# Performance work log

Hardware: AMD Instinct MI355X
Metric: run time of the kernel (lower is better)

The kernel has to match this reference:

```python
import jax, jax.numpy as jnp
import numpy as np

N, E = 50000, 800000
DIM_IN, DIM_H, DIM_OUT, HEADS = 128, 32, 16, 4
HID = DIM_H * HEADS  # 128
FINAL = DIM_OUT * HEADS  # 64
NEG_SLOPE = 0.2


def _glorot(key, shape):
    fan_in, fan_out = shape[0], shape[-1] if len(shape) > 1 else shape[0]
    lim = jnp.sqrt(6.0 / (fan_in + fan_out)).astype(jnp.float32)
    return jax.random.uniform(key, shape, jnp.float32, -lim, lim)


def setup_inputs() -> dict:
    key = jax.random.key(0)
    ks = jax.random.split(key, 16)
    x = jax.random.normal(ks[0], (N, DIM_IN), jnp.float32)
    edge_index = jax.random.randint(ks[1], (2, E), 0, N, dtype=jnp.int64)
    inp = {"x": x, "edge_index": edge_index}
    # layer 1: DIM_IN -> HEADS*DIM_H
    inp["Wl1"] = _glorot(ks[2], (DIM_IN, HEADS * DIM_H))
    inp["Wr1"] = _glorot(ks[3], (DIM_IN, HEADS * DIM_H))
    inp["att1"] = _glorot(ks[4], (HEADS, DIM_H))
    inp["b1"] = jnp.zeros((HEADS * DIM_H,), jnp.float32)
    # layer 2: HID -> HEADS*DIM_H
    inp["Wl2"] = _glorot(ks[5], (HID, HEADS * DIM_H))
    inp["Wr2"] = _glorot(ks[6], (HID, HEADS * DIM_H))
    inp["att2"] = _glorot(ks[7], (HEADS, DIM_H))
    inp["b2"] = jnp.zeros((HEADS * DIM_H,), jnp.float32)
    # layer 3: HID -> HEADS*DIM_OUT
    inp["Wl3"] = _glorot(ks[8], (HID, HEADS * DIM_OUT))
    inp["Wr3"] = _glorot(ks[9], (HID, HEADS * DIM_OUT))
    inp["att3"] = _glorot(ks[10], (HEADS, DIM_OUT))
    inp["b3"] = jnp.zeros((HEADS * DIM_OUT,), jnp.float32)
    return inp


def gatv2_conv(x, src, dst, Wl, Wr, att, b, heads, ch):
    n = x.shape[0]
    xl = (x @ Wl).reshape(n, heads, ch)  # source-side transform
    xr = (x @ Wr).reshape(n, heads, ch)  # target-side transform
    m = xl[src] + xr[dst]                 # [E, H, C]
    e = jnp.einsum('ehc,hc->eh', jax.nn.leaky_relu(m, NEG_SLOPE), att)
    # segment softmax over incoming edges of each dst node
    emax = jax.ops.segment_max(e, dst, num_segments=n)
    ex = jnp.exp(e - emax[dst])
    denom = jax.ops.segment_sum(ex, dst, num_segments=n)
    alpha = ex / denom[dst]               # [E, H]
    out = jax.ops.segment_sum(alpha[:, :, None] * xl[src], dst, num_segments=n)
    return out.reshape(n, heads * ch) + b


def reference(x, edge_index, Wl1, Wr1, att1, b1, Wl2, Wr2, att2, b2, Wl3, Wr3, att3, b3):
    n = x.shape[0]
    loops = jnp.arange(n, dtype=edge_index.dtype)
    src = jnp.concatenate([edge_index[0], loops])  # PyG add_self_loops=True
    dst = jnp.concatenate([edge_index[1], loops])
    # dropout is identity in eval mode
    h = jax.nn.elu(gatv2_conv(x, src, dst, Wl1, Wr1, att1, b1, HEADS, DIM_H))
    h = jax.nn.elu(gatv2_conv(h, src, dst, Wl2, Wr2, att2, b2, HEADS, DIM_H))
    h = gatv2_conv(h, src, dst, Wl3, Wr3, att3, b3, HEADS, DIM_OUT)
    return jax.nn.log_softmax(h, axis=1)
```

## Files before the change

kernel.cpp:

```cpp
#include <hip/hip_runtime.h>
#include <math.h>

constexpr int DIN  = 128;
constexpr int FSH  = 10;
constexpr int NFBM = 64;
constexpr int LCAP = 160;
constexpr int RND  = 4096;
constexpr int FCAP = 18432;

typedef __attribute__((ext_vector_type(8))) short short8;
typedef __attribute__((ext_vector_type(4))) float f32x4;

__device__ __forceinline__ unsigned short f2bf(float f) {
  unsigned u = __float_as_uint(f);
  u = (u + 0x7FFF + ((u >> 16) & 1)) >> 16;
  return (unsigned short)u;
}
__device__ __forceinline__ float bflo(unsigned u) { return __uint_as_float(u << 16); }
__device__ __forceinline__ float bfhi(unsigned u) { return __uint_as_float(u & 0xFFFF0000u); }

__device__ __forceinline__ void unpack8(uint4 u, float* x) {
  x[0] = bflo(u.x); x[1] = bfhi(u.x); x[2] = bflo(u.y); x[3] = bfhi(u.y);
  x[4] = bflo(u.z); x[5] = bfhi(u.z); x[6] = bflo(u.w); x[7] = bfhi(u.w);
}
__device__ __forceinline__ void unpack4(uint2 u, float* x) {
  x[0] = bflo(u.x); x[1] = bfhi(u.x); x[2] = bflo(u.y); x[3] = bfhi(u.y);
}

typedef const __attribute__((address_space(1))) unsigned int guint_t;
typedef __attribute__((address_space(3))) unsigned int luint_t;
__device__ __forceinline__ void async16(const void* g, void* l) {
  __builtin_amdgcn_global_load_lds((guint_t*)g, (luint_t*)l, 16, 0, 0);
}


__global__ __launch_bounds__(256) void bucket_append_kernel(const int* __restrict__ ei,
    int* __restrict__ gcnt, unsigned* __restrict__ gpairs, int E, int nfb) {
  __shared__ unsigned buf[NFBM * LCAP];
  __shared__ int cnt[NFBM];
  __shared__ int gbase[NFBM];
  const int tid = threadIdx.x;
  if (tid < NFBM) cnt[tid] = 0;
  __syncthreads();

  const int k0 = blockIdx.x * RND;
  for (int i = tid; i < RND; i += 256) {
    int k = k0 + i;
    if (k >= E) break;
    int src = ei[k], dst = ei[E + k];
    int fb = dst >> FSH;
    int pos = atomicAdd(&cnt[fb], 1);
    if (pos < LCAP)
      buf[fb * LCAP + pos] = (unsigned)src | ((unsigned)(dst & ((1 << FSH) - 1)) << 16);
  }
  __syncthreads();

  if (tid < nfb) gbase[tid] = atomicAdd(&gcnt[tid], min(cnt[tid], LCAP));
  __syncthreads();

  const int wid = tid >> 6, lane = tid & 63;
  for (int fb = wid; fb < nfb; fb += 4) {
    int c  = min(cnt[fb], LCAP);
    int gb = gbase[fb];
    if (gb >= FCAP) continue;
    c = min(c, FCAP - gb);
    unsigned* dstp = gpairs + (size_t)fb * FCAP + gb;
    const unsigned* srcp = &buf[fb * LCAP];
    for (int i = lane; i < c; i += 64) dstp[i] = srcp[i];
  }
}

__global__ __launch_bounds__(256) void bucket_build_kernel(const unsigned* __restrict__ gpairs,
    const int* __restrict__ gcnt, int* __restrict__ row_ptr,
    int* __restrict__ edge_src, int n, int nfb) {
  const int b   = blockIdx.x;
  const int tid = threadIdx.x;
  const int lane = tid & 63, wid = tid >> 6;
  __shared__ int hist[1024];
  __shared__ int wsum[4];
  __shared__ int base_s;

  const int d0 = b << FSH;
  const int nvalid = min(1 << FSH, n - d0);

  if (tid == 0) {
    int s = 0;
    for (int i = 0; i < b; ++i)
      s += min(gcnt[i], FCAP) + min(1 << FSH, n - (i << FSH));
    base_s = s;
  }
  for (int i = tid; i < 1024; i += 256) hist[i] = (i < nvalid) ? 1 : 0;
  __syncthreads();

  const int cnt = min(gcnt[b], FCAP);
  const unsigned* bp = gpairs + (size_t)b * FCAP;
  for (int i = tid; i < cnt; i += 256)
    atomicAdd(&hist[bp[i] >> 16], 1);
  __syncthreads();

  const int i4 = tid * 4;
  int h0 = hist[i4], h1 = hist[i4 + 1], h2 = hist[i4 + 2], h3 = hist[i4 + 3];
  int s = h0 + h1 + h2 + h3;
  int incl = s;
#pragma unroll
  for (int o = 1; o < 64; o <<= 1) {
    int t = __shfl_up(incl, o, 64);
    if (lane >= o) incl += t;
  }
  if (lane == 63) wsum[wid] = incl;
  __syncthreads();
  int wo = 0;
  for (int wq = 0; wq < wid; ++wq) wo += wsum[wq];
  const int base = base_s;
  int ex[4];
  ex[0] = wo + incl - s;
  ex[1] = ex[0] + h0;
  ex[2] = ex[1] + h1;
  ex[3] = ex[2] + h2;
#pragma unroll
  for (int j = 0; j < 4; ++j) {
    int d = i4 + j;
    if (d < nvalid) {
      row_ptr[d0 + d] = base + ex[j];
      edge_src[base + ex[j]] = d0 + d;
      hist[d] = ex[j] + 1;
    } else if (d0 + d == n) {
      row_ptr[n] = base + ex[j];
    }
  }
  if (b == nfb - 1 && d0 + 1024 <= n && tid == 0) row_ptr[n] = base + cnt + nvalid;
  __syncthreads();

  for (int i = tid; i < cnt; i += 256) {
    unsigned p = bp[i];
    int pos = atomicAdd(&hist[p >> 16], 1);
    edge_src[base + pos] = (int)(p & 0xFFFFu);
  }
}


__global__ __launch_bounds__(256) void cvt_x_kernel(const float* __restrict__ x,
                                                    unsigned short* __restrict__ xb, int total4) {
  int i = blockIdx.x * 256 + threadIdx.x;
  if (i >= total4) return;
  float4 v = *(const float4*)&x[i * 4];
  uint2 o;
  o.x = (unsigned)f2bf(v.x) | ((unsigned)f2bf(v.y) << 16);
  o.y = (unsigned)f2bf(v.z) | ((unsigned)f2bf(v.w) << 16);
  *(uint2*)&xb[i * 4] = o;
}

__global__ __launch_bounds__(256) void cvt_w_kernel(
    const float* __restrict__ Wl1, const float* __restrict__ Wr1,
    const float* __restrict__ Wl2, const float* __restrict__ Wr2,
    const float* __restrict__ Wl3, const float* __restrict__ Wr3,
    unsigned short* __restrict__ Wt) {
  int e = blockIdx.x * 256 + threadIdx.x;
  if (e >= 81920) return;
  const float* src; int N; int off;
  if (e < 65536) {
    int m = e >> 14; off = e & 16383; N = 128;
    src = (m == 0) ? Wl1 : (m == 1) ? Wr1 : (m == 2) ? Wl2 : Wr2;
  } else {
    int e2 = e - 65536; int m = e2 >> 13; off = e2 & 8191; N = 64;
    src = m ? Wr3 : Wl3;
  }
  int nn = off >> 7, k = off & 127;
  Wt[e] = f2bf(src[(size_t)k * N + nn]);
}


template<int NC>
__global__ __launch_bounds__(256) void gemm2_mfma(const unsigned short* __restrict__ A,
    const unsigned short* __restrict__ Wlt, const unsigned short* __restrict__ Wrt,
    unsigned short* __restrict__ outl, unsigned short* __restrict__ outr, int M) {
  constexpr int WNB = NC / 16;
  __shared__ char lds[16384 + NC * 256];
  char* As = lds;
  char* Ws = lds + 16384;
  const int tid  = threadIdx.x;
  const int w    = tid >> 6, lane = tid & 63;
  const int q    = lane >> 4, r15 = lane & 15;
  const int row0 = blockIdx.x * 64;

  {
    int r = row0 + w * 16 + r15; if (r >= M) r = M - 1;
    const char* g = (const char*)A + (size_t)r * 256 + q * 16;
    char* l = As + w * 4096;
#pragma unroll
    for (int kk = 0; kk < 4; ++kk) async16(g + kk * 64, l + kk * 1024);
  }
  for (int nt = w; nt < WNB; nt += 4) {
    const char* g = (const char*)Wlt + ((size_t)(nt * 16 + r15)) * 256 + q * 16;
    char* l = Ws + nt * 4096;
#pragma unroll
    for (int kk = 0; kk < 4; ++kk) async16(g + kk * 64, l + kk * 1024);
  }
  __syncthreads();

  const char* aw = As + w * 4096;
  f32x4 acc[WNB] = {};
#pragma unroll
  for (int kk = 0; kk < 4; ++kk) {
    short8 af = *(const short8*)(aw + kk * 1024 + (size_t)lane * 16);
#pragma unroll
    for (int nt = 0; nt < WNB; ++nt) {
      short8 bf = *(const short8*)(Ws + (nt * 4 + kk) * 1024 + (size_t)lane * 16);
      acc[nt] = __builtin_amdgcn_mfma_f32_16x16x32_bf16(af, bf, acc[nt], 0, 0, 0);
    }
  }
  {
    int rowb = row0 + w * 16 + q * 4;
#pragma unroll
    for (int nt = 0; nt < WNB; ++nt)
#pragma unroll
      for (int r = 0; r < 4; ++r) {
        int rr = rowb + r;
        if (rr < M) outl[(size_t)rr * NC + nt * 16 + r15] = f2bf(acc[nt][r]);
      }
  }
  __syncthreads();
  for (int nt = w; nt < WNB; nt += 4) {
    const char* g = (const char*)Wrt + ((size_t)(nt * 16 + r15)) * 256 + q * 16;
    char* l = Ws + nt * 4096;
#pragma unroll
    for (int kk = 0; kk < 4; ++kk) async16(g + kk * 64, l + kk * 1024);
  }
  __syncthreads();

  f32x4 acc2[WNB] = {};
#pragma unroll
  for (int kk = 0; kk < 4; ++kk) {
    short8 af = *(const short8*)(aw + kk * 1024 + (size_t)lane * 16);
#pragma unroll
    for (int nt = 0; nt < WNB; ++nt) {
      short8 bf = *(const short8*)(Ws + (nt * 4 + kk) * 1024 + (size_t)lane * 16);
      acc2[nt] = __builtin_amdgcn_mfma_f32_16x16x32_bf16(af, bf, acc2[nt], 0, 0, 0);
    }
  }
  {
    int rowb = row0 + w * 16 + q * 4;
#pragma unroll
    for (int nt = 0; nt < WNB; ++nt)
#pragma unroll
      for (int r = 0; r < 4; ++r) {
        int rr = rowb + r;
        if (rr < M) outr[(size_t)rr * NC + nt * 16 + r15] = f2bf(acc2[nt][r]);
      }
  }
}


__global__ __launch_bounds__(256) void aggregate128_kernel(
    const unsigned short* __restrict__ xl, const unsigned short* __restrict__ xr,
    const float* __restrict__ att, const float* __restrict__ bias,
    const int* __restrict__ row_ptr, const int* __restrict__ edge_src,
    unsigned short* __restrict__ out, int n) {
  const int tid  = threadIdx.x;
  const int r    = tid & 15;
  const int node = blockIdx.x * 16 + (tid >> 4);
  if (node >= n) return;
  const int c0 = r * 8;

  float xrv[8];
  unpack8(*(const uint4*)&xr[(size_t)node * 128 + c0], xrv);
  float a6[8], a4[8];
  {
    float4 aa = *(const float4*)&att[c0];
    float4 ab = *(const float4*)&att[c0 + 4];
    float at[8] = {aa.x, aa.y, aa.z, aa.w, ab.x, ab.y, ab.z, ab.w};
#pragma unroll
    for (int j = 0; j < 8; ++j) { a6[j] = 0.6f * at[j]; a4[j] = 0.4f * at[j]; }
  }

  float l = 0.f, o[8] = {};
  int idx = row_ptr[node];
  const int end = row_ptr[node + 1];

  for (; idx + 2 <= end; idx += 2) {
    int s0 = edge_src[idx], s1 = edge_src[idx + 1];
    uint4 u0 = *(const uint4*)&xl[(size_t)s0 * 128 + c0];
    uint4 u1 = *(const uint4*)&xl[(size_t)s1 * 128 + c0];
    float x0[8], x1[8];
    unpack8(u0, x0); unpack8(u1, x1);
    float p0 = 0.f, p1 = 0.f;
#pragma unroll
    for (int j = 0; j < 8; ++j) {
      float t = x0[j] + xrv[j];
      p0 = fmaf(t, a6[j], p0); p0 = fmaf(fabsf(t), a4[j], p0);
    }
#pragma unroll
    for (int j = 0; j < 8; ++j) {
      float t = x1[j] + xrv[j];
      p1 = fmaf(t, a6[j], p1); p1 = fmaf(fabsf(t), a4[j], p1);
    }
    p0 += __shfl_xor(p0, 1, 64); p0 += __shfl_xor(p0, 2, 64);
    p1 += __shfl_xor(p1, 1, 64); p1 += __shfl_xor(p1, 2, 64);
    float e0 = __expf(fminf(p0, 80.f));
    float e1 = __expf(fminf(p1, 80.f));
    l += e0 + e1;
#pragma unroll
    for (int j = 0; j < 8; ++j) o[j] = fmaf(e0, x0[j], fmaf(e1, x1[j], o[j]));
  }
  if (idx < end) {
    int s0 = edge_src[idx];
    uint4 u0 = *(const uint4*)&xl[(size_t)s0 * 128 + c0];
    float x0[8];
    unpack8(u0, x0);
    float p0 = 0.f;
#pragma unroll
    for (int j = 0; j < 8; ++j) {
      float t = x0[j] + xrv[j];
      p0 = fmaf(t, a6[j], p0); p0 = fmaf(fabsf(t), a4[j], p0);
    }
    p0 += __shfl_xor(p0, 1, 64); p0 += __shfl_xor(p0, 2, 64);
    float e0 = __expf(fminf(p0, 80.f));
    l += e0;
#pragma unroll
    for (int j = 0; j < 8; ++j) o[j] = fmaf(e0, x0[j], o[j]);
  }

  float4 b0 = *(const float4*)&bias[c0];
  float4 b1 = *(const float4*)&bias[c0 + 4];
  float bb[8] = {b0.x, b0.y, b0.z, b0.w, b1.x, b1.y, b1.z, b1.w};
  unsigned short res[8];
#pragma unroll
  for (int j = 0; j < 8; ++j) {
    float v = o[j] / l + bb[j];
    v = v > 0.f ? v : __expf(v) - 1.f;
    res[j] = f2bf(v);
  }
  uint4 ov;
  ov.x = (unsigned)res[0] | ((unsigned)res[1] << 16);
  ov.y = (unsigned)res[2] | ((unsigned)res[3] << 16);
  ov.z = (unsigned)res[4] | ((unsigned)res[5] << 16);
  ov.w = (unsigned)res[6] | ((unsigned)res[7] << 16);
  *(uint4*)&out[(size_t)node * 128 + c0] = ov;
}


__global__ __launch_bounds__(256) void aggregate64_kernel(
    const unsigned short* __restrict__ xl, const unsigned short* __restrict__ xr,
    const float* __restrict__ att, const float* __restrict__ bias,
    const int* __restrict__ row_ptr, const int* __restrict__ edge_src,
    float* __restrict__ out, int n) {
  const int tid  = threadIdx.x;
  const int r    = tid & 15;
  const int node = blockIdx.x * 16 + (tid >> 4);
  if (node >= n) return;
  const int c0 = r * 4;

  float xrv[4];
  unpack4(*(const uint2*)&xr[(size_t)node * 64 + c0], xrv);
  float a6[4], a4[4];
  {
    float4 aa = *(const float4*)&att[c0];
    float at[4] = {aa.x, aa.y, aa.z, aa.w};
#pragma unroll
    for (int j = 0; j < 4; ++j) { a6[j] = 0.6f * at[j]; a4[j] = 0.4f * at[j]; }
  }

  float l = 0.f, o[4] = {};
  int idx = row_ptr[node];
  const int end = row_ptr[node + 1];

  for (; idx + 2 <= end; idx += 2) {
    int s0 = edge_src[idx], s1 = edge_src[idx + 1];
    uint2 u0 = *(const uint2*)&xl[(size_t)s0 * 64 + c0];
    uint2 u1 = *(const uint2*)&xl[(size_t)s1 * 64 + c0];
    float x0[4], x1[4];
    unpack4(u0, x0); unpack4(u1, x1);
    float p0 = 0.f, p1 = 0.f;
#pragma unroll
    for (int j = 0; j < 4; ++j) {
      float t = x0[j] + xrv[j];
      p0 = fmaf(t, a6[j], p0); p0 = fmaf(fabsf(t), a4[j], p0);
    }
#pragma unroll
    for (int j = 0; j < 4; ++j) {
      float t = x1[j] + xrv[j];
      p1 = fmaf(t, a6[j], p1); p1 = fmaf(fabsf(t), a4[j], p1);
    }
    p0 += __shfl_xor(p0, 1, 64); p0 += __shfl_xor(p0, 2, 64);
    p1 += __shfl_xor(p1, 1, 64); p1 += __shfl_xor(p1, 2, 64);
    float e0 = __expf(fminf(p0, 80.f));
    float e1 = __expf(fminf(p1, 80.f));
    l += e0 + e1;
#pragma unroll
    for (int j = 0; j < 4; ++j) o[j] = fmaf(e0, x0[j], fmaf(e1, x1[j], o[j]));
  }
  if (idx < end) {
    int s0 = edge_src[idx];
    uint2 u0 = *(const uint2*)&xl[(size_t)s0 * 64 + c0];
    float x0[4];
    unpack4(u0, x0);
    float p0 = 0.f;
#pragma unroll
    for (int j = 0; j < 4; ++j) {
      float t = x0[j] + xrv[j];
      p0 = fmaf(t, a6[j], p0); p0 = fmaf(fabsf(t), a4[j], p0);
    }
    p0 += __shfl_xor(p0, 1, 64); p0 += __shfl_xor(p0, 2, 64);
    float e0 = __expf(fminf(p0, 80.f));
    l += e0;
#pragma unroll
    for (int j = 0; j < 4; ++j) o[j] = fmaf(e0, x0[j], o[j]);
  }

  float4 bv = *(const float4*)&bias[c0];
  float bb[4] = {bv.x, bv.y, bv.z, bv.w};
  float rr[4];
#pragma unroll
  for (int j = 0; j < 4; ++j) rr[j] = o[j] / l + bb[j];

  float mx = fmaxf(fmaxf(rr[0], rr[1]), fmaxf(rr[2], rr[3]));
#pragma unroll
  for (int off = 1; off < 16; off <<= 1) mx = fmaxf(mx, __shfl_xor(mx, off, 64));
  float se = __expf(rr[0] - mx) + __expf(rr[1] - mx) +
             __expf(rr[2] - mx) + __expf(rr[3] - mx);
#pragma unroll
  for (int off = 1; off < 16; off <<= 1) se += __shfl_xor(se, off, 64);
  float ls = mx + __logf(se);
  *(float4*)&out[(size_t)node * 64 + c0] =
      make_float4(rr[0] - ls, rr[1] - ls, rr[2] - ls, rr[3] - ls);
}


extern "C" void kernel_launch(void* const* d_in, const int* in_sizes, int n_in,
                              void* d_out, int out_size, void* d_ws, size_t ws_size,
                              hipStream_t stream) {
  const float* x    = (const float*)d_in[0];
  const int*   ei   = (const int*)d_in[1];
  const float* Wl1  = (const float*)d_in[2];
  const float* Wr1  = (const float*)d_in[3];
  const float* att1 = (const float*)d_in[4];
  const float* b1   = (const float*)d_in[5];
  const float* Wl2  = (const float*)d_in[6];
  const float* Wr2  = (const float*)d_in[7];
  const float* att2 = (const float*)d_in[8];
  const float* b2   = (const float*)d_in[9];
  const float* Wl3  = (const float*)d_in[10];
  const float* Wr3  = (const float*)d_in[11];
  const float* att3 = (const float*)d_in[12];
  const float* b3   = (const float*)d_in[13];
  const int n = in_sizes[0] / DIN;
  const int E = in_sizes[1] / 2;
  float* out = (float*)d_out;

  const int nfb = (n + (1 << FSH) - 1) >> FSH;

  unsigned short* xb = (unsigned short*)d_ws;
  unsigned short* xl = xb + (size_t)n * 128;
  unsigned short* xr = xl + (size_t)n * 128;
  unsigned short* h  = xr + (size_t)n * 128;
  unsigned short* Wt = h + (size_t)n * 128;
  unsigned short* Wl1t = Wt, *Wr1t = Wt + 16384;
  unsigned short* Wl2t = Wt + 32768, *Wr2t = Wt + 49152;
  unsigned short* Wl3t = Wt + 65536, *Wr3t = Wt + 73728;
  int* row_ptr  = (int*)(Wt + 81920);
  int* gcnt     = row_ptr + (n + 16);
  int* edge_src = gcnt + NFBM;
  unsigned* gpairs = (unsigned*)(edge_src + (((size_t)E + n + 15) & ~(size_t)15));

  cvt_w_kernel<<<320, 256, 0, stream>>>(Wl1, Wr1, Wl2, Wr2, Wl3, Wr3, Wt);
  cvt_x_kernel<<<(n * 128 / 4 + 255) / 256, 256, 0, stream>>>(x, xb, n * 128 / 4);

  hipMemsetAsync(gcnt, 0, NFBM * sizeof(int), stream);
  bucket_append_kernel<<<(E + RND - 1) / RND, 256, 0, stream>>>(ei, gcnt, gpairs, E, nfb);
  bucket_build_kernel<<<nfb, 256, 0, stream>>>(gpairs, gcnt, row_ptr, edge_src, n, nfb);

  const int gb = (n + 63) / 64;
  const int ab = (n + 15) / 16;

  gemm2_mfma<128><<<gb, 256, 0, stream>>>(xb, Wl1t, Wr1t, xl, xr, n);
  aggregate128_kernel<<<ab, 256, 0, stream>>>(xl, xr, att1, b1, row_ptr, edge_src, h, n);
  gemm2_mfma<128><<<gb, 256, 0, stream>>>(h, Wl2t, Wr2t, xl, xr, n);
  aggregate128_kernel<<<ab, 256, 0, stream>>>(xl, xr, att2, b2, row_ptr, edge_src, h, n);
  gemm2_mfma<64><<<gb, 256, 0, stream>>>(h, Wl3t, Wr3t, xl, xr, n);
  aggregate64_kernel<<<ab, 256, 0, stream>>>(xl, xr, att3, b3, row_ptr, edge_src, out, n);
}
```

Baseline: 310.0 us.

## Fuse x bf16 conversion into first GEMM, unroll aggregation by four, parallelize bucket prefix

The first-layer GEMM now reads fp32 x directly and converts it to bf16 while storing it to LDS in the swizzled layout. This removes the separate conversion kernel and its global round trip. The aggregation kernels process four edges per iteration instead of two to expose more independent gathers. The bucket base offset is computed with a wavefront reduction instead of a serial loop in one thread. The CVT path swaps async copies for synchronous loads, and the wider unroll increases register pressure.

Result: faster. 298.3 us (-3.8%).

```diff
diff --git a/kernel.cpp b/kernel.cpp
--- a/kernel.cpp
+++ b/kernel.cpp
@@ -83,11 +83,13 @@
   const int d0 = b << FSH;
   const int nvalid = min(1 << FSH, n - d0);
 
-  if (tid == 0) {
-    int s = 0;
-    for (int i = 0; i < b; ++i)
-      s += min(gcnt[i], FCAP) + min(1 << FSH, n - (i << FSH));
-    base_s = s;
+  if (wid == 0) {
+    int term = 0;
+    if (lane < b)
+      term = min(gcnt[lane], FCAP) + min(1 << FSH, n - (lane << FSH));
+#pragma unroll
+    for (int o = 32; o >= 1; o >>= 1) term += __shfl_xor(term, o, 64);
+    if (lane == 0) base_s = term;
   }
   for (int i = tid; i < 1024; i += 256) hist[i] = (i < nvalid) ? 1 : 0;
   __syncthreads();
@@ -136,18 +138,6 @@
     int pos = atomicAdd(&hist[p >> 16], 1);
     edge_src[base + pos] = (int)(p & 0xFFFFu);
   }
-}
-
-
-__global__ __launch_bounds__(256) void cvt_x_kernel(const float* __restrict__ x,
-                                                    unsigned short* __restrict__ xb, int total4) {
-  int i = blockIdx.x * 256 + threadIdx.x;
-  if (i >= total4) return;
-  float4 v = *(const float4*)&x[i * 4];
-  uint2 o;
-  o.x = (unsigned)f2bf(v.x) | ((unsigned)f2bf(v.y) << 16);
-  o.y = (unsigned)f2bf(v.z) | ((unsigned)f2bf(v.w) << 16);
-  *(uint2*)&xb[i * 4] = o;
 }
 
 __global__ __launch_bounds__(256) void cvt_w_kernel(
@@ -170,8 +160,8 @@
 }
 
 
-template<int NC>
-__global__ __launch_bounds__(256) void gemm2_mfma(const unsigned short* __restrict__ A,
+template<int NC, bool CVT>
+__global__ __launch_bounds__(256) void gemm2_mfma(const void* __restrict__ Ap,
     const unsigned short* __restrict__ Wlt, const unsigned short* __restrict__ Wrt,
     unsigned short* __restrict__ outl, unsigned short* __restrict__ outr, int M) {
   constexpr int WNB = NC / 16;
@@ -183,7 +173,21 @@
   const int q    = lane >> 4, r15 = lane & 15;
   const int row0 = blockIdx.x * 64;
 
-  {
+  if constexpr (CVT) {
+    const float* Af = (const float*)Ap;
+    for (int idx = tid * 4; idx < 64 * 128; idx += 1024) {
+      int rl = idx >> 7, k = idx & 127;
+      int rg = row0 + rl; if (rg >= M) rg = M - 1;
+      float4 v = *(const float4*)&Af[(size_t)rg * 128 + k];
+      uint2 pk;
+      pk.x = (unsigned)f2bf(v.x) | ((unsigned)f2bf(v.y) << 16);
+      pk.y = (unsigned)f2bf(v.z) | ((unsigned)f2bf(v.w) << 16);
+      char* addr = As + (rl >> 4) * 4096 + (k >> 5) * 1024 +
+                   ((((k >> 3) & 3) * 16) + (rl & 15)) * 16 + (k & 7) * 2;
+      *(uint2*)addr = pk;
+    }
+  } else {
+    const unsigned short* A = (const unsigned short*)Ap;
     int r = row0 + w * 16 + r15; if (r >= M) r = M - 1;
     const char* g = (const char*)A + (size_t)r * 256 + q * 16;
     char* l = As + w * 4096;
@@ -277,32 +281,37 @@
   int idx = row_ptr[node];
   const int end = row_ptr[node + 1];
 
-  for (; idx + 2 <= end; idx += 2) {
-    int s0 = edge_src[idx], s1 = edge_src[idx + 1];
+  for (; idx + 4 <= end; idx += 4) {
+    int s0 = edge_src[idx],     s1 = edge_src[idx + 1];
+    int s2 = edge_src[idx + 2], s3 = edge_src[idx + 3];
     uint4 u0 = *(const uint4*)&xl[(size_t)s0 * 128 + c0];
     uint4 u1 = *(const uint4*)&xl[(size_t)s1 * 128 + c0];
-    float x0[8], x1[8];
-    unpack8(u0, x0); unpack8(u1, x1);
-    float p0 = 0.f, p1 = 0.f;
+    uint4 u2 = *(const uint4*)&xl[(size_t)s2 * 128 + c0];
+    uint4 u3 = *(const uint4*)&xl[(size_t)s3 * 128 + c0];
+    float x0[8], x1[8], x2[8], x3[8];
+    unpack8(u0, x0); unpack8(u1, x1); unpack8(u2, x2); unpack8(u3, x3);
+    float p0 = 0.f, p1 = 0.f, p2 = 0.f, p3 = 0.f;
 #pragma unroll
     for (int j = 0; j < 8; ++j) {
-      float t = x0[j] + xrv[j];
-      p0 = fmaf(t, a6[j], p0); p0 = fmaf(fabsf(t), a4[j], p0);
-    }
-#pragma unroll
-    for (int j = 0; j < 8; ++j) {
-      float t = x1[j] + xrv[j];
-      p1 = fmaf(t, a6[j], p1); p1 = fmaf(fabsf(t), a4[j], p1);
+      float t0 = x0[j] + xrv[j], t1 = x1[j] + xrv[j];
+      float t2 = x2[j] + xrv[j], t3 = x3[j] + xrv[j];
+      p0 = fmaf(t0, a6[j], p0); p0 = fmaf(fabsf(t0), a4[j], p0);
+      p1 = fmaf(t1, a6[j], p1); p1 = fmaf(fabsf(t1), a4[j], p1);
+      p2 = fmaf(t2, a6[j], p2); p2 = fmaf(fabsf(t2), a4[j], p2);
+      p3 = fmaf(t3, a6[j], p3); p3 = fmaf(fabsf(t3), a4[j], p3);
     }
     p0 += __shfl_xor(p0, 1, 64); p0 += __shfl_xor(p0, 2, 64);
     p1 += __shfl_xor(p1, 1, 64); p1 += __shfl_xor(p1, 2, 64);
-    float e0 = __expf(fminf(p0, 80.f));
-    float e1 = __expf(fminf(p1, 80.f));
-    l += e0 + e1;
-#pragma unroll
-    for (int j = 0; j < 8; ++j) o[j] = fmaf(e0, x0[j], fmaf(e1, x1[j], o[j]));
-  }
-  if (idx < end) {
+    p2 += __shfl_xor(p2, 1, 64); p2 += __shfl_xor(p2, 2, 64);
+    p3 += __shfl_xor(p3, 1, 64); p3 += __shfl_xor(p3, 2, 64);
+    float e0 = __expf(fminf(p0, 80.f)), e1 = __expf(fminf(p1, 80.f));
+    float e2 = __expf(fminf(p2, 80.f)), e3 = __expf(fminf(p3, 80.f));
+    l += (e0 + e1) + (e2 + e3);
+#pragma unroll
+    for (int j = 0; j < 8; ++j)
+      o[j] = fmaf(e0, x0[j], fmaf(e1, x1[j], fmaf(e2, x2[j], fmaf(e3, x3[j], o[j]))));
+  }
+  for (; idx < end; ++idx) {
     int s0 = edge_src[idx];
     uint4 u0 = *(const uint4*)&xl[(size_t)s0 * 128 + c0];
     float x0[8];
@@ -364,32 +373,37 @@
   int idx = row_ptr[node];
   const int end = row_ptr[node + 1];
 
-  for (; idx + 2 <= end; idx += 2) {
-    int s0 = edge_src[idx], s1 = edge_src[idx + 1];
+  for (; idx + 4 <= end; idx += 4) {
+    int s0 = edge_src[idx],     s1 = edge_src[idx + 1];
+    int s2 = edge_src[idx + 2], s3 = edge_src[idx + 3];
     uint2 u0 = *(const uint2*)&xl[(size_t)s0 * 64 + c0];
     uint2 u1 = *(const uint2*)&xl[(size_t)s1 * 64 + c0];
-    float x0[4], x1[4];
-    unpack4(u0, x0); unpack4(u1, x1);
-    float p0 = 0.f, p1 = 0.f;
+    uint2 u2 = *(const uint2*)&xl[(size_t)s2 * 64 + c0];
+    uint2 u3 = *(const uint2*)&xl[(size_t)s3 * 64 + c0];
+    float x0[4], x1[4], x2[4], x3[4];
+    unpack4(u0, x0); unpack4(u1, x1); unpack4(u2, x2); unpack4(u3, x3);
+    float p0 = 0.f, p1 = 0.f, p2 = 0.f, p3 = 0.f;
 #pragma unroll
     for (int j = 0; j < 4; ++j) {
-      float t = x0[j] + xrv[j];
-      p0 = fmaf(t, a6[j], p0); p0 = fmaf(fabsf(t), a4[j], p0);
-    }
-#pragma unroll
-    for (int j = 0; j < 4; ++j) {
-      float t = x1[j] + xrv[j];
-      p1 = fmaf(t, a6[j], p1); p1 = fmaf(fabsf(t), a4[j], p1);
+      float t0 = x0[j] + xrv[j], t1 = x1[j] + xrv[j];
+      float t2 = x2[j] + xrv[j], t3 = x3[j] + xrv[j];
+      p0 = fmaf(t0, a6[j], p0); p0 = fmaf(fabsf(t0), a4[j], p0);
+      p1 = fmaf(t1, a6[j], p1); p1 = fmaf(fabsf(t1), a4[j], p1);
+      p2 = fmaf(t2, a6[j], p2); p2 = fmaf(fabsf(t2), a4[j], p2);
+      p3 = fmaf(t3, a6[j], p3); p3 = fmaf(fabsf(t3), a4[j], p3);
     }
     p0 += __shfl_xor(p0, 1, 64); p0 += __shfl_xor(p0, 2, 64);
     p1 += __shfl_xor(p1, 1, 64); p1 += __shfl_xor(p1, 2, 64);
-    float e0 = __expf(fminf(p0, 80.f));
-    float e1 = __expf(fminf(p1, 80.f));
-    l += e0 + e1;
-#pragma unroll
-    for (int j = 0; j < 4; ++j) o[j] = fmaf(e0, x0[j], fmaf(e1, x1[j], o[j]));
-  }
-  if (idx < end) {
+    p2 += __shfl_xor(p2, 1, 64); p2 += __shfl_xor(p2, 2, 64);
+    p3 += __shfl_xor(p3, 1, 64); p3 += __shfl_xor(p3, 2, 64);
+    float e0 = __expf(fminf(p0, 80.f)), e1 = __expf(fminf(p1, 80.f));
+    float e2 = __expf(fminf(p2, 80.f)), e3 = __expf(fminf(p3, 80.f));
+    l += (e0 + e1) + (e2 + e3);
+#pragma unroll
+    for (int j = 0; j < 4; ++j)
+      o[j] = fmaf(e0, x0[j], fmaf(e1, x1[j], fmaf(e2, x2[j], fmaf(e3, x3[j], o[j]))));
+  }
+  for (; idx < end; ++idx) {
     int s0 = edge_src[idx];
     uint2 u0 = *(const uint2*)&xl[(size_t)s0 * 64 + c0];
     float x0[4];
@@ -449,8 +463,7 @@
 
   const int nfb = (n + (1 << FSH) - 1) >> FSH;
 
-  unsigned short* xb = (unsigned short*)d_ws;
-  unsigned short* xl = xb + (size_t)n * 128;
+  unsigned short* xl = (unsigned short*)d_ws;
   unsigned short* xr = xl + (size_t)n * 128;
   unsigned short* h  = xr + (size_t)n * 128;
   unsigned short* Wt = h + (size_t)n * 128;
@@ -463,7 +476,6 @@
   unsigned* gpairs = (unsigned*)(edge_src + (((size_t)E + n + 15) & ~(size_t)15));
 
   cvt_w_kernel<<<320, 256, 0, stream>>>(Wl1, Wr1, Wl2, Wr2, Wl3, Wr3, Wt);
-  cvt_x_kernel<<<(n * 128 / 4 + 255) / 256, 256, 0, stream>>>(x, xb, n * 128 / 4);
 
   hipMemsetAsync(gcnt, 0, NFBM * sizeof(int), stream);
   bucket_append_kernel<<<(E + RND - 1) / RND, 256, 0, stream>>>(ei, gcnt, gpairs, E, nfb);
@@ -472,10 +484,10 @@
   const int gb = (n + 63) / 64;
   const int ab = (n + 15) / 16;
 
-  gemm2_mfma<128><<<gb, 256, 0, stream>>>(xb, Wl1t, Wr1t, xl, xr, n);
+  gemm2_mfma<128, true><<<gb, 256, 0, stream>>>(x, Wl1t, Wr1t, xl, xr, n);
   aggregate128_kernel<<<ab, 256, 0, stream>>>(xl, xr, att1, b1, row_ptr, edge_src, h, n);
-  gemm2_mfma<128><<<gb, 256, 0, stream>>>(h, Wl2t, Wr2t, xl, xr, n);
+  gemm2_mfma<128, false><<<gb, 256, 0, stream>>>(h, Wl2t, Wr2t, xl, xr, n);
   aggregate128_kernel<<<ab, 256, 0, stream>>>(xl, xr, att2, b2, row_ptr, edge_src, h, n);
-  gemm2_mfma<64><<<gb, 256, 0, stream>>>(h, Wl3t, Wr3t, xl, xr, n);
+  gemm2_mfma<64, false><<<gb, 256, 0, stream>>>(h, Wl3t, Wr3t, xl, xr, n);
   aggregate64_kernel<<<ab, 256, 0, stream>>>(xl, xr, att3, b3, row_ptr, edge_src, out, n);
 }
```
